# Performance work log

Hardware: AMD Instinct MI355X
Metric: run time of the kernel (lower is better)

The kernel has to match this reference:

```python
import jax, jax.numpy as jnp
import numpy as np

N = 50000
E = 1_600_000
S = 0.05  # param init scale


def setup_inputs() -> dict:
    key = jax.random.key(0)
    ks = jax.random.split(key, 12)
    return {
        "x": jax.random.normal(ks[0], (N, 1), jnp.float32),
        "edge_index": jax.random.randint(ks[1], (2, E), 0, N, dtype=jnp.int32),
        "W_gcn": jax.random.normal(ks[2], (2, 128), jnp.float32) * S,
        "b_gcn": jax.random.normal(ks[3], (128,), jnp.float32) * S,
        "W_sage_l": jax.random.normal(ks[4], (128, 128), jnp.float32) * S,
        "b_sage_l": jax.random.normal(ks[5], (128,), jnp.float32) * S,
        "W_sage_r": jax.random.normal(ks[6], (128, 128), jnp.float32) * S,
        "W_v1": jax.random.normal(ks[7], (128, 64), jnp.float32) * S,
        "b_v1": jax.random.normal(ks[8], (64,), jnp.float32) * S,
        "W_v2": jax.random.normal(ks[9], (64, 1), jnp.float32) * S,
        "b_v2": jax.random.normal(ks[10], (1,), jnp.float32) * S,
    }


def reference(x, edge_index, W_gcn, b_gcn, W_sage_l, b_sage_l, W_sage_r,
              W_v1, b_v1, W_v2, b_v2):
    n = x.shape[0]
    src, dst = edge_index[0], edge_index[1]
    ones_e = jnp.ones(src.shape, x.dtype)

    # degree feature: out-degree of source nodes (torch_geometric.utils.degree)
    deg0 = jax.ops.segment_sum(ones_e, src, num_segments=n)
    xin = jnp.concatenate([x, deg0[:, None]], axis=-1)  # [N, 2]

    # --- GCNConv(2,128): add self-loops, symmetric normalization ---
    loop = jnp.arange(n, dtype=src.dtype)
    s2 = jnp.concatenate([src, loop])
    d2 = jnp.concatenate([dst, loop])
    deg = jax.ops.segment_sum(jnp.ones(d2.shape, x.dtype), d2, num_segments=n)
    dinv = jnp.where(deg > 0, jax.lax.rsqrt(deg), 0.0)
    h = xin @ W_gcn                      # [N, 128]
    norm = dinv[s2] * dinv[d2]           # [E+N]
    z1 = jax.ops.segment_sum(norm[:, None] * h[s2], d2, num_segments=n) + b_gcn
    a1 = jax.nn.relu(z1)

    # --- SAGEConv(128,128): mean neighbor aggregation + root weight ---
    cnt = jax.ops.segment_sum(ones_e, dst, num_segments=n)
    agg = jax.ops.segment_sum(a1[src], dst, num_segments=n)
    agg = agg / jnp.maximum(cnt, 1.0)[:, None]
    a2 = agg @ W_sage_l + b_sage_l + a1 @ W_sage_r

    # --- value head ---
    v = jax.nn.relu(a2 @ W_v1 + b_v1) @ W_v2 + b_v2  # [N, 1]
    return jnp.sum(v)
```

## Files before the change

### kernel.cpp

```cpp
#include <hip/hip_runtime.h>

#define NCH 128
#define TILE 2048
#define CAP 10240
#define SCHUNK 2048
#define SNODES 32
#define HSTRIDE 264

typedef __attribute__((ext_vector_type(8))) short bf16x8;
typedef __attribute__((ext_vector_type(4))) float f32x4;

__device__ inline unsigned short f2bf(float f) {
  unsigned int u = __builtin_bit_cast(unsigned int, f);
  unsigned int r = u + 0x7fffu + ((u >> 16) & 1u);
  return (unsigned short)(r >> 16);
}

__global__ void prep_w_kernel(const float* __restrict__ Wl, const float* __restrict__ Wr,
                              const float* __restrict__ Wv1,
                              unsigned short* fw1, unsigned short* fw2,
                              int* __restrict__ gcur1, int* __restrict__ gcur2,
                              float* out, const float* __restrict__ bv2, int n) {
  int i = blockIdx.x * blockDim.x + threadIdx.x;
  if (i < 32768) {
    int j = i & 7, l = (i >> 3) & 63, s = (i >> 9) & 7, t = i >> 12;
    int k = s * 32 + (l >> 4) * 8 + j;
    int nn = t * 16 + (l & 15);
    float v = (k < 128) ? Wl[k * 128 + nn] : Wr[(k - 128) * 128 + nn];
    fw1[i] = f2bf(v);
  }
  if (i < 8192) {
    int j = i & 7, l = (i >> 3) & 63, s = (i >> 9) & 3, t = i >> 11;
    int k = s * 32 + (l >> 4) * 8 + j;
    int nn = t * 16 + (l & 15);
    fw2[i] = f2bf(Wv1[k * 64 + nn]);
  }
  if (i < 256) gcur1[i] = i * CAP;
  else if (i < 512) gcur2[i - 256] = (i - 256) * CAP;
  if (i == 512) out[0] = (float)n * bv2[0];
}

__global__ __launch_bounds__(256) void partition_kernel(
    const int* __restrict__ src, const int* __restrict__ dst,
    int* __restrict__ gcur1, int* __restrict__ gcur2,
    unsigned int* __restrict__ part, unsigned short* __restrict__ part_s, int ne) {
  __shared__ int h1[256], h2[256], c1[256], c2[256];
  int t = threadIdx.x, b = blockIdx.x;
  h1[t] = 0; h2[t] = 0;
  __syncthreads();
  int base = b * TILE;
  int lim = min(base + TILE, ne);
  for (int i = base + t; i < lim; i += 256) {
    atomicAdd(&h1[((unsigned)dst[i]) >> 8], 1);
    atomicAdd(&h2[((unsigned)src[i]) >> 8], 1);
  }
  __syncthreads();
  c1[t] = atomicAdd(&gcur1[t], h1[t]);
  c2[t] = atomicAdd(&gcur2[t], h2[t]);
  __syncthreads();
  for (int i = base + t; i < lim; i += 256) {
    unsigned d = (unsigned)dst[i], s = (unsigned)src[i];
    int p1 = atomicAdd(&c1[d >> 8], 1);
    part[p1] = (d << 16) | s;
    int p2 = atomicAdd(&c2[s >> 8], 1);
    part_s[p2] = (unsigned short)s;
  }
}

__global__ __launch_bounds__(256) void bucket_kernel(
    const unsigned int* __restrict__ part, const unsigned short* __restrict__ part_s,
    const int* __restrict__ gcur1, const int* __restrict__ gcur2,
    int* __restrict__ row_beg, int* __restrict__ deg, int* __restrict__ csr_src,
    const float* __restrict__ x, float* __restrict__ p2, int n) {
  __shared__ int h[256], h2[256], sc[256], c[256];
  int t = threadIdx.x;
  int b = blockIdx.x;
  h[t] = 0; h2[t] = 0;
  __syncthreads();
  int beg = b * CAP, end = gcur1[b];
  for (int i = beg + t; i < end; i += 256)
    atomicAdd(&h[(part[i] >> 16) & 255], 1);
  int sbeg = b * CAP, send = gcur2[b];
  for (int i = sbeg + t; i < send; i += 256)
    atomicAdd(&h2[part_s[i] & 255], 1);
  __syncthreads();
  int hv = h[t];
  sc[t] = hv;
  __syncthreads();
  for (int off = 1; off < 256; off <<= 1) {
    int u = (t >= off) ? sc[t - off] : 0;
    __syncthreads();
    sc[t] += u;
    __syncthreads();
  }
  int excl = sc[t] - hv;
  int node = b * 256 + t;
  if (node < n) { row_beg[node] = beg + excl; deg[node] = hv; }
  c[t] = beg + excl;
  __syncthreads();
  for (int i = beg + t; i < end; i += 256) {
    unsigned key = part[i];
    int pos = atomicAdd(&c[(key >> 16) & 255], 1);
    csr_src[pos] = (int)(key & 0xFFFFu);
  }
  if (node < n) {
    float dinv = rsqrtf((float)hv + 1.0f);
    p2[2 * node]     = dinv * x[node];
    p2[2 * node + 1] = dinv * (float)h2[t];
  }
}

__global__ __launch_bounds__(256) void gcn_t_kernel(
    const int* __restrict__ row_beg, const int* __restrict__ deg,
    const int* __restrict__ csr_src,
    const float* __restrict__ p2, float2* __restrict__ tvec, int npad, int n) {
  int wid = (blockIdx.x * blockDim.x + threadIdx.x) >> 6;
  int lane = threadIdx.x & 63;
  if (wid >= npad) return;
  if (wid >= n) { if (lane == 0) tvec[wid] = make_float2(0.f, 0.f); return; }
  int beg = row_beg[wid], dg = deg[wid], end = beg + dg;
  float s0 = 0.0f, s1 = 0.0f;
  for (int k = beg + lane; k < end; k += 64) {
    int s = csr_src[k];
    float2 v = *reinterpret_cast<const float2*>(p2 + 2 * (size_t)s);
    s0 += v.x; s1 += v.y;
  }
#pragma unroll
  for (int off = 1; off < 64; off <<= 1) {
    s0 += __shfl_xor(s0, off, 64);
    s1 += __shfl_xor(s1, off, 64);
  }
  float dinv = rsqrtf((float)dg + 1.0f);
  float2 self = *reinterpret_cast<const float2*>(p2 + 2 * (size_t)wid);
  if (lane == 0)
    tvec[wid] = make_float2(dinv * (s0 + self.x), dinv * (s1 + self.y));
}

__global__ __launch_bounds__(256) void sage_kernel(
    const int* __restrict__ row_beg, const int* __restrict__ deg,
    const int* __restrict__ csr_src, const float2* __restrict__ tvec,
    const float* __restrict__ Wg, const float* __restrict__ bg,
    unsigned int* __restrict__ agg32, int n) {
  __shared__ float2 sE[SCHUNK];
  __shared__ int sR[SNODES + 1];
  int tid = threadIdx.x, lane = tid & 63, w = tid >> 6;
  int node0 = blockIdx.x * SNODES;
  if (tid <= SNODES) {
    int node = node0 + tid;
    int v;
    if (node < n) v = row_beg[node];
    else v = row_beg[n - 1] + deg[n - 1];
    if (tid == SNODES && node - 1 < n)
      v = row_beg[node - 1] + deg[node - 1];
    sR[tid] = v;
  }
  __syncthreads();
  int base = sR[0], endAll = sR[SNODES];

  int c0 = 2 * lane, c1 = c0 + 1;
  float w00 = Wg[c0], w10 = Wg[NCH + c0], b0 = bg[c0];
  float w01 = Wg[c1], w11 = Wg[NCH + c1], b1 = bg[c1];
  float ax[8], ay[8];
#pragma unroll
  for (int i = 0; i < 8; i++) { ax[i] = 0.f; ay[i] = 0.f; }

  for (int cbeg = base; cbeg < endAll; cbeg += SCHUNK) {
    int cend = min(cbeg + SCHUNK, endAll);
    __syncthreads();
    for (int k = cbeg + tid; k < cend; k += 256)
      sE[k - cbeg] = tvec[csr_src[k]];
    __syncthreads();
#pragma unroll
    for (int i = 0; i < 8; i++) {
      int nd = w * 8 + i;
      int rb = max(sR[nd], cbeg) - cbeg;
      int re = min(sR[nd + 1], cend) - cbeg;
      int k = rb;
      for (; k + 3 < re; k += 4) {
        float2 tA = sE[k], tB = sE[k + 1], tC = sE[k + 2], tD = sE[k + 3];
        ax[i] += fmaxf(fmaf(tA.x, w00, fmaf(tA.y, w10, b0)), 0.f)
               + fmaxf(fmaf(tB.x, w00, fmaf(tB.y, w10, b0)), 0.f)
               + fmaxf(fmaf(tC.x, w00, fmaf(tC.y, w10, b0)), 0.f)
               + fmaxf(fmaf(tD.x, w00, fmaf(tD.y, w10, b0)), 0.f);
        ay[i] += fmaxf(fmaf(tA.x, w01, fmaf(tA.y, w11, b1)), 0.f)
               + fmaxf(fmaf(tB.x, w01, fmaf(tB.y, w11, b1)), 0.f)
               + fmaxf(fmaf(tC.x, w01, fmaf(tC.y, w11, b1)), 0.f)
               + fmaxf(fmaf(tD.x, w01, fmaf(tD.y, w11, b1)), 0.f);
      }
      for (; k < re; k++) {
        float2 tA = sE[k];
        ax[i] += fmaxf(fmaf(tA.x, w00, fmaf(tA.y, w10, b0)), 0.f);
        ay[i] += fmaxf(fmaf(tA.x, w01, fmaf(tA.y, w11, b1)), 0.f);
      }
    }
  }
#pragma unroll
  for (int i = 0; i < 8; i++) {
    int nd = w * 8 + i;
    int cnt = sR[nd + 1] - sR[nd];
    float inv = 1.0f / (float)(cnt > 1 ? cnt : 1);
    agg32[(size_t)(node0 + nd) * 64 + lane] =
        (unsigned int)f2bf(ax[i] * inv) | ((unsigned int)f2bf(ay[i] * inv) << 16);
  }
}

__global__ __launch_bounds__(256) void head_kernel(
    const unsigned short* __restrict__ agg, const float2* __restrict__ tvec,
    const float* __restrict__ Wg, const float* __restrict__ bg,
    const unsigned short* __restrict__ fw1, const unsigned short* __restrict__ fw2,
    const float* __restrict__ bl, const float* __restrict__ bv1,
    const float* __restrict__ Wv2, float* __restrict__ out, int n) {
  __shared__ __align__(16) unsigned short sA[64 * HSTRIDE];
  __shared__ float sT[128];
  __shared__ float sRed[4];
  int tid = threadIdx.x;
  int lane = tid & 63;
  int w = tid >> 6;
  int m16 = lane & 15;
  int quad = lane >> 4;
  int node0 = blockIdx.x * 64;

  const uint4* g = reinterpret_cast<const uint4*>(agg + (size_t)node0 * NCH);
  for (int c = tid; c < 1024; c += 256) {
    int row = c >> 4, off = c & 15;
    *reinterpret_cast<uint4*>(&sA[row * HSTRIDE + off * 8]) = g[row * 16 + off];
  }
  if (tid < 128) sT[tid] = reinterpret_cast<const float*>(tvec + node0)[tid];
  __syncthreads();

  {
    int cp = tid & 63, r0 = tid >> 6;
    int c0 = 2 * cp, c1 = c0 + 1;
    float w00 = Wg[c0], w10 = Wg[NCH + c0], b0 = bg[c0];
    float w01 = Wg[c1], w11 = Wg[NCH + c1], b1 = bg[c1];
#pragma unroll
    for (int i = 0; i < 16; i++) {
      int row = r0 + 4 * i;
      float t0 = sT[2 * row], t1 = sT[2 * row + 1];
      float z0 = fmaxf(fmaf(t0, w00, fmaf(t1, w10, b0)), 0.f);
      float z1 = fmaxf(fmaf(t0, w01, fmaf(t1, w11, b1)), 0.f);
      *reinterpret_cast<unsigned int*>(&sA[row * HSTRIDE + 128 + 2 * cp]) =
          (unsigned int)f2bf(z0) | ((unsigned int)f2bf(z1) << 16);
    }
  }

  bf16x8 b1f[2][8];
  const bf16x8* f1 = reinterpret_cast<const bf16x8*>(fw1);
#pragma unroll
  for (int p = 0; p < 2; p++)
#pragma unroll
    for (int s = 0; s < 8; s++)
      b1f[p][s] = f1[((w * 2 + p) * 8 + s) * 64 + lane];

  f32x4 acc[4][2];
#pragma unroll
  for (int mt = 0; mt < 4; mt++)
#pragma unroll
    for (int p = 0; p < 2; p++) acc[mt][p] = (f32x4)0.0f;

  __syncthreads();

#pragma unroll
  for (int s = 0; s < 8; s++) {
#pragma unroll
    for (int mt = 0; mt < 4; mt++) {
      bf16x8 aF = *reinterpret_cast<const bf16x8*>(
          &sA[(mt * 16 + m16) * HSTRIDE + s * 32 + quad * 8]);
#pragma unroll
      for (int p = 0; p < 2; p++)
        acc[mt][p] = __builtin_amdgcn_mfma_f32_16x16x32_bf16(aF, b1f[p][s],
                                                             acc[mt][p], 0, 0, 0);
    }
  }

  float blv[2];
#pragma unroll
  for (int p = 0; p < 2; p++) blv[p] = bl[(w * 2 + p) * 16 + m16];
  __syncthreads();
#pragma unroll
  for (int mt = 0; mt < 4; mt++)
#pragma unroll
    for (int p = 0; p < 2; p++) {
      int col = (w * 2 + p) * 16 + m16;
#pragma unroll
      for (int r = 0; r < 4; r++) {
        int row = mt * 16 + quad * 4 + r;
        sA[row * HSTRIDE + col] = f2bf(acc[mt][p][r] + blv[p]);
      }
    }
  __syncthreads();

  bf16x8 b2f[4];
  const bf16x8* f2 = reinterpret_cast<const bf16x8*>(fw2);
#pragma unroll
  for (int s = 0; s < 4; s++) b2f[s] = f2[(w * 4 + s) * 64 + lane];

  f32x4 acc2[4];
#pragma unroll
  for (int mt = 0; mt < 4; mt++) acc2[mt] = (f32x4)0.0f;

#pragma unroll
  for (int s = 0; s < 4; s++) {
#pragma unroll
    for (int mt = 0; mt < 4; mt++) {
      bf16x8 aF = *reinterpret_cast<const bf16x8*>(
          &sA[(mt * 16 + m16) * HSTRIDE + s * 32 + quad * 8]);
      acc2[mt] = __builtin_amdgcn_mfma_f32_16x16x32_bf16(aF, b2f[s], acc2[mt], 0, 0, 0);
    }
  }

  int c2 = w * 16 + m16;
  float bvj = bv1[c2], w2 = Wv2[c2];
  float vsum = 0.0f;
#pragma unroll
  for (int mt = 0; mt < 4; mt++)
#pragma unroll
    for (int r = 0; r < 4; r++) {
      int node = node0 + mt * 16 + quad * 4 + r;
      if (node < n) vsum += fmaxf(acc2[mt][r] + bvj, 0.0f) * w2;
    }
#pragma unroll
  for (int off = 1; off < 64; off <<= 1) vsum += __shfl_xor(vsum, off, 64);
  if (lane == 0) sRed[w] = vsum;
  __syncthreads();
  if (tid == 0) atomicAdd(out, sRed[0] + sRed[1] + sRed[2] + sRed[3]);
}

extern "C" void kernel_launch(void* const* d_in, const int* in_sizes, int n_in,
                              void* d_out, int out_size, void* d_ws, size_t ws_size,
                              hipStream_t stream) {
  const float* x   = (const float*)d_in[0];
  const int*   ei  = (const int*)d_in[1];
  const float* Wg  = (const float*)d_in[2];
  const float* bg  = (const float*)d_in[3];
  const float* Wl  = (const float*)d_in[4];
  const float* bl  = (const float*)d_in[5];
  const float* Wr  = (const float*)d_in[6];
  const float* Wv1 = (const float*)d_in[7];
  const float* bv1 = (const float*)d_in[8];
  const float* Wv2 = (const float*)d_in[9];
  const float* bv2 = (const float*)d_in[10];
  float* out = (float*)d_out;

  int n  = in_sizes[0];
  int E_ = in_sizes[1] / 2;
  int npad = ((n + 63) / 64) * 64;
  int B1 = (E_ + TILE - 1) / TILE;
  const int* src = ei;
  const int* dst = ei + E_;

  char* base = (char*)d_ws;
  unsigned short* agg = (unsigned short*)base;  base += (size_t)npad * NCH * 2;
  float2* tvec    = (float2*)base;              base += (size_t)npad * 8;
  unsigned short* fw1 = (unsigned short*)base;  base += 32768 * 2;
  unsigned short* fw2 = (unsigned short*)base;  base += 8192 * 2;
  float* p2       = (float*)base;               base += (size_t)n * 2 * 4;
  int* gcur1      = (int*)base;                 base += 256 * 4;
  int* gcur2      = (int*)base;                 base += 256 * 4;
  unsigned int* part = (unsigned int*)base;     base += (size_t)256 * CAP * 4;
  int* row_beg    = (int*)base;                 base += (size_t)n * 4;
  int* deg        = (int*)base;                 base += (size_t)n * 4;
  int* csr_src    = (int*)base;                 base += (size_t)E_ * 4;
  unsigned short* part_s = (unsigned short*)base;

  prep_w_kernel<<<128, 256, 0, stream>>>(Wl, Wr, Wv1, fw1, fw2, gcur1, gcur2,
                                         out, bv2, n);
  partition_kernel<<<B1, 256, 0, stream>>>(src, dst, gcur1, gcur2, part, part_s, E_);
  bucket_kernel<<<256, 256, 0, stream>>>(part, part_s, gcur1, gcur2,
                                         row_beg, deg, csr_src, x, p2, n);

  int wave_blocks = npad / 4;
  gcn_t_kernel<<<wave_blocks, 256, 0, stream>>>(row_beg, deg, csr_src, p2,
                                                tvec, npad, n);
  sage_kernel<<<npad / SNODES, 256, 0, stream>>>(row_beg, deg, csr_src, tvec,
                                                 Wg, bg, (unsigned int*)agg, n);
  head_kernel<<<npad / 64, 256, 0, stream>>>(agg, tvec, Wg, bg, fw1, fw2,
                                             bl, bv1, Wv2, out, n);
}
```

Measured before the change: 218.5 us.

## Split partition bucket counters per XCD to cut cross-die atomic contention

The edge partitioning now keeps separate bucket cursors and sub-regions for each of the 8 XCDs, chosen with the hardware XCC_ID register. This keeps the global atomicAdds on bucket cursors within one die. The bucket kernel then walks all 8 sub-buckets to build each CSR bucket, and bucket output bases become fixed at b*8192. The cost is more small strided loops in bucket_kernel, a larger workspace, and a fixed per-bucket capacity assumption that could overflow on skewed inputs.

```diff
diff --git a/kernel.cpp b/kernel.cpp
--- a/kernel.cpp
+++ b/kernel.cpp
@@ -2,7 +2,7 @@
 
 #define NCH 128
 #define TILE 2048
-#define CAP 10240
+#define SUBCAP 3072
 #define SCHUNK 2048
 #define SNODES 32
 #define HSTRIDE 264
@@ -14,6 +14,12 @@
   unsigned int u = __builtin_bit_cast(unsigned int, f);
   unsigned int r = u + 0x7fffu + ((u >> 16) & 1u);
   return (unsigned short)(r >> 16);
+}
+
+__device__ inline int xcc_id() {
+  int x;
+  asm volatile("s_getreg_b32 %0, hwreg(HW_REG_XCC_ID)" : "=s"(x));
+  return x & 7;
 }
 
 __global__ void prep_w_kernel(const float* __restrict__ Wl, const float* __restrict__ Wr,
@@ -35,9 +41,9 @@
     int nn = t * 16 + (l & 15);
     fw2[i] = f2bf(Wv1[k * 64 + nn]);
   }
-  if (i < 256) gcur1[i] = i * CAP;
-  else if (i < 512) gcur2[i - 256] = (i - 256) * CAP;
-  if (i == 512) out[0] = (float)n * bv2[0];
+  if (i < 2048) gcur1[i] = i * SUBCAP;
+  else if (i < 4096) gcur2[i - 2048] = (i - 2048) * SUBCAP;
+  if (i == 4096) out[0] = (float)n * bv2[0];
 }
 
 __global__ __launch_bounds__(256) void partition_kernel(
@@ -55,8 +61,9 @@
     atomicAdd(&h2[((unsigned)src[i]) >> 8], 1);
   }
   __syncthreads();
-  c1[t] = atomicAdd(&gcur1[t], h1[t]);
-  c2[t] = atomicAdd(&gcur2[t], h2[t]);
+  int xcd = xcc_id();
+  c1[t] = atomicAdd(&gcur1[xcd * 256 + t], h1[t]);
+  c2[t] = atomicAdd(&gcur2[xcd * 256 + t], h2[t]);
   __syncthreads();
   for (int i = base + t; i < lim; i += 256) {
     unsigned d = (unsigned)dst[i], s = (unsigned)src[i];
@@ -73,16 +80,21 @@
     int* __restrict__ row_beg, int* __restrict__ deg, int* __restrict__ csr_src,
     const float* __restrict__ x, float* __restrict__ p2, int n) {
   __shared__ int h[256], h2[256], sc[256], c[256];
+  __shared__ int outBase;
   int t = threadIdx.x;
   int b = blockIdx.x;
   h[t] = 0; h2[t] = 0;
-  __syncthreads();
-  int beg = b * CAP, end = gcur1[b];
-  for (int i = beg + t; i < end; i += 256)
-    atomicAdd(&h[(part[i] >> 16) & 255], 1);
-  int sbeg = b * CAP, send = gcur2[b];
-  for (int i = sbeg + t; i < send; i += 256)
-    atomicAdd(&h2[part_s[i] & 255], 1);
+  if (t == 0) outBase = 0;
+  __syncthreads();
+#pragma unroll
+  for (int xz = 0; xz < 8; xz++) {
+    int rb = (xz * 256 + b) * SUBCAP, re = gcur1[xz * 256 + b];
+    for (int i = rb + t; i < re; i += 256)
+      atomicAdd(&h[(part[i] >> 16) & 255], 1);
+    int sb = (xz * 256 + b) * SUBCAP, se = gcur2[xz * 256 + b];
+    for (int i = sb + t; i < se; i += 256)
+      atomicAdd(&h2[part_s[i] & 255], 1);
+  }
   __syncthreads();
   int hv = h[t];
   sc[t] = hv;
@@ -93,15 +105,20 @@
     sc[t] += u;
     __syncthreads();
   }
+  int bucketBase = b * 8192;
   int excl = sc[t] - hv;
   int node = b * 256 + t;
-  if (node < n) { row_beg[node] = beg + excl; deg[node] = hv; }
-  c[t] = beg + excl;
-  __syncthreads();
-  for (int i = beg + t; i < end; i += 256) {
-    unsigned key = part[i];
-    int pos = atomicAdd(&c[(key >> 16) & 255], 1);
-    csr_src[pos] = (int)(key & 0xFFFFu);
+  if (node < n) { row_beg[node] = bucketBase + excl; deg[node] = hv; }
+  c[t] = bucketBase + excl;
+  __syncthreads();
+#pragma unroll
+  for (int xz = 0; xz < 8; xz++) {
+    int rb = (xz * 256 + b) * SUBCAP, re = gcur1[xz * 256 + b];
+    for (int i = rb + t; i < re; i += 256) {
+      unsigned key = part[i];
+      int pos = atomicAdd(&c[(key >> 16) & 255], 1);
+      csr_src[pos] = (int)(key & 0xFFFFu);
+    }
   }
   if (node < n) {
     float dinv = rsqrtf((float)hv + 1.0f);
@@ -148,10 +165,14 @@
   if (tid <= SNODES) {
     int node = node0 + tid;
     int v;
-    if (node < n) v = row_beg[node];
-    else v = row_beg[n - 1] + deg[n - 1];
-    if (tid == SNODES && node - 1 < n)
-      v = row_beg[node - 1] + deg[node - 1];
+    if (tid == SNODES) {
+      int last = min(node, n) - 1;
+      v = (last >= 0) ? row_beg[last] + deg[last] : 0;
+    } else if (node < n) {
+      v = row_beg[node];
+    } else {
+      v = (n > 0) ? row_beg[n - 1] + deg[n - 1] : 0;
+    }
     sR[tid] = v;
   }
   __syncthreads();
@@ -355,12 +376,12 @@
   unsigned short* fw1 = (unsigned short*)base;  base += 32768 * 2;
   unsigned short* fw2 = (unsigned short*)base;  base += 8192 * 2;
   float* p2       = (float*)base;               base += (size_t)n * 2 * 4;
-  int* gcur1      = (int*)base;                 base += 256 * 4;
-  int* gcur2      = (int*)base;                 base += 256 * 4;
-  unsigned int* part = (unsigned int*)base;     base += (size_t)256 * CAP * 4;
+  int* gcur1      = (int*)base;                 base += 2048 * 4;
+  int* gcur2      = (int*)base;                 base += 2048 * 4;
+  unsigned int* part = (unsigned int*)base;     base += (size_t)2048 * SUBCAP * 4;
   int* row_beg    = (int*)base;                 base += (size_t)n * 4;
   int* deg        = (int*)base;                 base += (size_t)n * 4;
-  int* csr_src    = (int*)base;                 base += (size_t)E_ * 4;
+  int* csr_src    = (int*)base;                 base += (size_t)256 * 8192 * 4;
   unsigned short* part_s = (unsigned short*)base;
 
   prep_w_kernel<<<128, 256, 0, stream>>>(Wl, Wr, Wv1, fw1, fw2, gcur1, gcur2,
```

Measured after the change: 205.7 us. 5.9% less time.
